# Performance work log

Hardware: AMD Instinct MI355X
Metric: run time of the kernel (lower is better)

Reference implementation:

```python
import jax, jax.numpy as jnp
import numpy as np

NUM_IT = 5            # init_kwargs num_it
N_NODES = 200_000
N_EDGES = 6_400_000   # avg degree 32
N_INIT_COLORS = 16

# odd 32-bit mixing constants (Knuth / xxhash primes); uint32 mults wrap mod 2^32
M1 = np.uint32(2654435761)
M2 = np.uint32(2246822519)
M3 = np.uint32(3266489917)
M4 = np.uint32(668265263)


def setup_inputs() -> dict:
    key = jax.random.key(0)
    k1, k2 = jax.random.split(key)
    x = jax.random.randint(k1, (N_NODES,), 0, N_INIT_COLORS, dtype=jnp.int32)
    edge_index = jax.random.randint(k2, (2, N_EDGES), 0, N_NODES, dtype=jnp.int32)
    return {"x": x, "edge_index": edge_index}


def _wl_iteration(colors, row, col, num_nodes):
    """One WLConv step: new color = id of (own color, sorted multiset of neighbor colors).

    The torch WLConv sorts each node's neighbor colors, hashes the tuple, and
    assigns compact ids via a dict. Here we do the same math vectorized:
    lexsort edges by (row, neighbor color), compute a position-weighted 2x32-bit
    hash of the sorted per-node sequence via segment_sum, mix in the node's own
    color, then relabel distinct keys to compact ids 0..k-1 with jnp.unique.
    """
    E = row.shape[0]
    c = colors[col]                                   # neighbor colors per edge [E]
    order = jnp.lexsort((c, row))                     # sort by node, then by color
    r_s = row[order]                                  # [E] sorted rows
    c_s = c[order].astype(jnp.uint32)                 # [E] sorted neighbor colors

    ones = jnp.ones((E,), dtype=jnp.int32)
    deg = jax.ops.segment_sum(ones, row, num_segments=num_nodes)      # [N]
    start = jnp.cumsum(deg) - deg                                     # segment offsets [N]
    pos = (jnp.arange(E, dtype=jnp.int32) - start[r_s]).astype(jnp.uint32)  # rank within node

    # two independent position-weighted hash lanes over each sorted neighbor list
    lane1 = jax.ops.segment_sum((c_s + 1) * (pos * M1 + M2), r_s, num_segments=num_nodes)
    lane2 = jax.ops.segment_sum((c_s + 1) * (pos * M3 + M4), r_s, num_segments=num_nodes)

    own = colors.astype(jnp.uint32) + 1
    key2 = jnp.stack([lane1 * M2 + own * M1, lane2 * M4 + own * M3], axis=1)  # [N,2]

    # dict-style relabeling: distinct keys -> compact ids (at most N distinct)
    _, inv = jnp.unique(key2, axis=0, size=num_nodes, return_inverse=True,
                        fill_value=jnp.uint32(0))
    return inv.reshape(-1).astype(colors.dtype)


def reference(x, edge_index):
    row, col = edge_index[0], edge_index[1]
    colors = x.astype(jnp.int32)
    for _ in range(NUM_IT):  # fixed small layer loop, not a data-dim loop
        colors = _wl_iteration(colors, row, col, N_NODES)
    return colors
```

## Files before the change

### kernel.cpp

```cpp
#include <hip/hip_runtime.h>
#include <stdint.h>

typedef unsigned int u32;
typedef unsigned long long u64;

#define M1 2654435761u
#define M2 2246822519u
#define M3 3266489917u
#define M4 668265263u
#define NUM_IT 5
#define PCHUNK 16384
#define HCH 65536
#define TILE 4096
#define PBCH 4096
#define CCAP 16384
#define SB 64
#define CHB 33
#define NKB 2048
#define KSH 53
#define KCH 4096
#define SCH 8192


__global__ void k_init(const int* __restrict__ x, int* __restrict__ colors,
                       u32* __restrict__ bcnt5, u32* __restrict__ bhist,
                       u32* __restrict__ cnt3, int n, int nbuck) {
    int i = blockIdx.x * blockDim.x + threadIdx.x;
    if (i < n) colors[i] = x[i];
    if (i < 2 * NUM_IT * NKB) bcnt5[i] = 0u;
    if (i >= 24576 && i < 24576 + nbuck) bhist[i - 24576] = 0u;
    if (i >= 32768 && i < 32768 + 48) cnt3[i - 32768] = 0u;
}

__global__ void k_chist(const int* __restrict__ row, u32* __restrict__ bhist,
                        u32* __restrict__ thist, int e, int nbuck) {
    __shared__ u32 fineh[1024];
    __shared__ u32 shist[16 * SB];
    int t = threadIdx.x;
    fineh[t] = 0u;
    shist[t] = 0u;
    __syncthreads();
    int c0 = blockIdx.x * HCH;
    int ce = c0 + HCH; if (ce > e) ce = e;
    int k = 0;
    for (int i = c0 + t; i < ce; i += 1024, ++k) {
        u32 r = (u32)row[i];
        atomicAdd(&fineh[r >> 8], 1u);
        atomicAdd(&shist[((k >> 2) << 6) | (r >> 12)], 1u);
    }
    __syncthreads();
    if (t < nbuck) {
        u32 v = fineh[t];
        if (v) atomicAdd(&bhist[t], v);
    }
    {
        int m = t >> 6;
        if (c0 + m * TILE < e)
            thist[(size_t)(blockIdx.x * 16 + m) * SB + (t & 63)] = shist[t];
    }
}

__global__ void k_cscan(const u32* __restrict__ bhist, u32* __restrict__ boffE,
                        u32* __restrict__ bcur, u32* __restrict__ boffS,
                        int nbuck, int nbS) {
    __shared__ u32 sh[256];
    u32 run = 0u;
    for (int base = 0; base < nbuck; base += 256) {
        int id = base + threadIdx.x;
        u32 x = (id < nbuck) ? bhist[id] : 0u;
        sh[threadIdx.x] = x;
        __syncthreads();
        for (int o = 1; o < 256; o <<= 1) {
            u32 t = (threadIdx.x >= (u32)o) ? sh[threadIdx.x - o] : 0u;
            __syncthreads();
            sh[threadIdx.x] += t;
            __syncthreads();
        }
        if (id < nbuck) {
            u32 excl = sh[threadIdx.x] - x + run;
            boffE[id] = excl;
            bcur[id] = excl;
            if ((id & 15) == 0) boffS[id >> 4] = excl;
        }
        u32 tot = sh[255];
        __syncthreads();
        run += tot;
    }
    if (threadIdx.x == 0) { boffE[nbuck] = run; boffS[nbS] = run; }
}

__global__ void k_tscan(const u32* __restrict__ thist, const u32* __restrict__ boffS,
                        u32* __restrict__ tbase, int ntiles) {
    __shared__ u32 sh[256];
    int b = blockIdx.x;
    int t = threadIdx.x;
    u32 run = boffS[b];
    for (int base = 0; base < ntiles; base += 256) {
        int tile = base + t;
        u32 x = (tile < ntiles) ? thist[(size_t)tile * SB + b] : 0u;
        sh[t] = x;
        __syncthreads();
        for (int o = 1; o < 256; o <<= 1) {
            u32 y = (t >= o) ? sh[t - o] : 0u;
            __syncthreads();
            sh[t] += y;
            __syncthreads();
        }
        if (tile < ntiles) tbase[(size_t)tile * SB + b] = run + sh[t] - x;
        u32 tot = sh[255];
        __syncthreads();
        run += tot;
    }
}

__global__ void k_partA(const int* __restrict__ row, const int* __restrict__ col,
                        const u32* __restrict__ thist, const u32* __restrict__ tbase,
                        u32* __restrict__ adjt, int e) {
    __shared__ u32 vals[TILE];
    __shared__ unsigned char bkt[TILE];
    __shared__ u32 lbase[SB + 1], gbase[SB], cur[SB];
    int t = threadIdx.x;
    int c0 = blockIdx.x * TILE;
    int ce = c0 + TILE; if (ce > e) ce = e;
    if (t < SB) {
        gbase[t] = tbase[(size_t)blockIdx.x * SB + t];
        cur[t] = 0u;
        lbase[t] = thist[(size_t)blockIdx.x * SB + t];
    }
    __syncthreads();
    if (t == 0) {
        u32 run = 0u;
        for (int b = 0; b < SB; ++b) { u32 h = lbase[b]; lbase[b] = run; run += h; }
        lbase[SB] = run;
    }
    __syncthreads();
    for (int i = c0 + t; i < ce; i += 256) {
        u32 r = (u32)row[i];
        u32 s = r >> 12;
        u32 p = lbase[s] + atomicAdd(&cur[s], 1u);
        vals[p] = ((r & 4095u) << 18) | (u32)col[i];
        bkt[p] = (unsigned char)s;
    }
    __syncthreads();
    int cnt = ce - c0;
    for (int i = t; i < cnt; i += 256) {
        u32 b = (u32)bkt[i];
        adjt[gbase[b] + ((u32)i - lbase[b])] = vals[i];
    }
}

__global__ void k_partB(const u32* __restrict__ adjt, const u32* __restrict__ boffS,
                        u32* __restrict__ ecur, u32* __restrict__ adj) {
    __shared__ u32 vals[PBCH];
    __shared__ u32 hist[16], lbase[17], gbase[16], cur[16];
    int s = blockIdx.x / CHB, c = blockIdx.x % CHB;
    u32 lo = boffS[s] + (u32)c * PBCH;
    u32 hi = boffS[s + 1];
    if (lo >= hi) return;
    if (hi > lo + PBCH) hi = lo + PBCH;
    int t = threadIdx.x;
    if (t < 16) hist[t] = 0u;
    __syncthreads();
    for (u32 i = lo + t; i < hi; i += 256)
        atomicAdd(&hist[(adjt[i] >> 26) & 15u], 1u);
    __syncthreads();
    if (t == 0) {
        u32 run = 0u;
        for (int b = 0; b < 16; ++b) { lbase[b] = run; run += hist[b]; }
        lbase[16] = run;
    }
    __syncthreads();
    if (t < 16) {
        u32 h = hist[t];
        gbase[t] = h ? atomicAdd(&ecur[s * 16 + t], h) : 0u;
        cur[t] = 0u;
    }
    __syncthreads();
    for (u32 i = lo + t; i < hi; i += 256) {
        u32 v = adjt[i];
        u32 b = (v >> 26) & 15u;
        vals[lbase[b] + atomicAdd(&cur[b], 1u)] = v;
    }
    __syncthreads();
    u32 cnt = hi - lo;
    for (u32 i = t; i < cnt; i += 256) {
        u32 v = vals[i];
        u32 b = (v >> 26) & 15u;
        adj[gbase[b] + (i - lbase[b])] = v & 0x03FFFFFFu;
    }
}

__global__ void k_part(const int* __restrict__ row, const int* __restrict__ col,
                       u32* __restrict__ bcur, u32* __restrict__ adjp, int e, int nbuck) {
    __shared__ u32 hist[1024], base[1024], cur[1024];
    int c0 = blockIdx.x * PCHUNK;
    int cend = c0 + PCHUNK; if (cend > e) cend = e;
    for (int t = threadIdx.x; t < nbuck; t += 256) hist[t] = 0u;
    __syncthreads();
    for (int i = c0 + threadIdx.x; i < cend; i += 256)
        atomicAdd(&hist[((u32)row[i]) >> 8], 1u);
    __syncthreads();
    for (int t = threadIdx.x; t < nbuck; t += 256) {
        u32 h = hist[t];
        base[t] = h ? atomicAdd(&bcur[t], h) : 0u;
        cur[t] = 0u;
    }
    __syncthreads();
    for (int i = c0 + threadIdx.x; i < cend; i += 256) {
        u32 r = (u32)row[i];
        u32 b = r >> 8;
        u32 local = atomicAdd(&cur[b], 1u);
        adjp[base[b] + local] = ((r & 255u) << 18) | (u32)col[i];
    }
}

__global__ void k_csr(u32* __restrict__ adj, const u32* __restrict__ boffE,
                      u32* __restrict__ deg, u32* __restrict__ start,
                      u64* __restrict__ lists, u32* __restrict__ cnt3, int n) {
    __shared__ u32 buf[CCAP];
    __shared__ u32 cnt[256], cur[256];
    __shared__ u32 wsum[4];
    __shared__ u32 ch[3], cbase[3];
    int b = blockIdx.x;
    int v0 = b << 8;
    u32 bs = boffE[b], be = boffE[b + 1];
    int c = (int)(be - bs);
    if (c > CCAP) c = CCAP;
    int t = threadIdx.x;
    int lane = t & 63, w = t >> 6;
    if (t < 256) cnt[t] = 0u;
    if (t < 3) ch[t] = 0u;
    for (int i = t; i < c; i += 1024) buf[i] = adj[bs + i];
    __syncthreads();
    for (int i = t; i < c; i += 1024)
        atomicAdd(&cnt[buf[i] >> 18], 1u);
    __syncthreads();
    u32 myc = 0u, ps = 0u;
    if (t < 256) {
        myc = cnt[t];
        ps = myc;
#pragma unroll
        for (int o = 1; o < 64; o <<= 1) {
            u32 y = (u32)__shfl_up((int)ps, o, 64);
            if (lane >= o) ps += y;
        }
        if (lane == 63) wsum[w] = ps;
    }
    __syncthreads();
    u32 cls = 0u, crk = 0u, myStart = 0u;
    int v = v0 + t;
    if (t < 256) {
        u32 wb = 0u;
        for (int j = 0; j < w; ++j) wb += wsum[j];
        u32 excl = wb + ps - myc;
        myStart = bs + excl;
        if (v < n) {
            deg[v] = myc;
            start[v] = myStart;
            cls = (myc <= 32u) ? 0u : ((myc <= 64u) ? 1u : 2u);
            crk = atomicAdd(&ch[cls], 1u);
        }
        cur[t] = myStart;
    }
    __syncthreads();
    if (t < 3) cbase[t] = ch[t] ? atomicAdd(&cnt3[t * 16], ch[t]) : 0u;
    __syncthreads();
    if (t < 256 && v < n) {
        u32 dcl = myc > 0x3FFFu ? 0x3FFFu : myc;
        lists[cls * (size_t)n + cbase[cls] + crk] =
            ((u64)((dcl << 18) | (u32)v) << 32) | (u64)myStart;
    }
    for (int i = t; i < c; i += 1024) {
        u32 p = buf[i];
        u32 q = atomicAdd(&cur[p >> 18], 1u);
        adj[q] = p & 0x3FFFFu;
    }
}


__device__ __forceinline__ void ce_reg(u32& a, u32& b, bool up) {
    u32 mn = a < b ? a : b, mx = a < b ? b : a;
    a = up ? mn : mx; b = up ? mx : mn;
}
__device__ __forceinline__ void ce_shf(u32& a, int o, bool tm) {
    u32 ot = (u32)__shfl_xor((int)a, o, 64);
    u32 mn = a < ot ? a : ot, mx = a < ot ? ot : a;
    a = tm ? mn : mx;
}
#define CE_SH4(o, tm) { ce_shf(c0, o, tm); ce_shf(c1, o, tm); ce_shf(c2, o, tm); ce_shf(c3, o, tm); }
#define CE_RG4(up)    { ce_reg(c0, c2, up); ce_reg(c1, c3, up); ce_reg(c0, c1, up); ce_reg(c2, c3, up); }

__global__ void k_hash(const int* __restrict__ colors, const u32* __restrict__ deg,
                       const u32* __restrict__ adj,
                       const u64* __restrict__ lists, const u32* __restrict__ cnt3,
                       u64* __restrict__ keys, int n) {
    int lane = threadIdx.x & 63;
    int wid = (int)((blockIdx.x * 256u + threadIdx.x) >> 6);
    u32 nA = cnt3[0], nBc = cnt3[16], nCc = cnt3[32];
    int octA = (int)((nA + 7u) >> 3);
    int quadB = (int)((nBc + 3u) >> 2);
    if (wid < octA) {
        int s = lane & 7;
        int li = 8 * wid + (lane >> 3);
        int node = -1;
        u32 c0 = 0xFFFFFFFFu, c1 = 0xFFFFFFFFu, c2 = 0xFFFFFFFFu, c3 = 0xFFFFFFFFu;
        u32 e0 = 4u * (u32)s;
        if (li < (int)nA) {
            u64 pk = lists[li];
            u32 st = (u32)pk;
            u32 hi = (u32)(pk >> 32);
            u32 d = hi >> 18;
            node = (int)(hi & 0x3FFFFu);
            if (e0 + 0u < d) c0 = (u32)colors[adj[st + e0 + 0u]];
            if (e0 + 1u < d) c1 = (u32)colors[adj[st + e0 + 1u]];
            if (e0 + 2u < d) c2 = (u32)colors[adj[st + e0 + 2u]];
            if (e0 + 3u < d) c3 = (u32)colors[adj[st + e0 + 3u]];
        }
        bool s1 = (s & 1) == 0, s2 = (s & 2) == 0, s4 = (s & 4) == 0;
        ce_reg(c0, c1, true); ce_reg(c2, c3, false);
        CE_RG4(s1)
        CE_SH4(1, s1 == s2)
        CE_RG4(s2)
        CE_SH4(2, s2 == s4)
        CE_SH4(1, s1 == s4)
        CE_RG4(s4)
        CE_SH4(4, s4)
        CE_SH4(2, s2)
        CE_SH4(1, s1)
        CE_RG4(true)
        u32 a1 = e0 * M1, a3 = e0 * M3;
        u32 v = (c0 + 1u) * (a1 + M2)           + (c1 + 1u) * (a1 + 1u * M1 + M2)
              + (c2 + 1u) * (a1 + 2u * M1 + M2) + (c3 + 1u) * (a1 + 3u * M1 + M2);
        u32 w = (c0 + 1u) * (a3 + M4)           + (c1 + 1u) * (a3 + 1u * M3 + M4)
              + (c2 + 1u) * (a3 + 2u * M3 + M4) + (c3 + 1u) * (a3 + 3u * M3 + M4);
#pragma unroll
        for (int o = 1; o < 8; o <<= 1) {
            v += (u32)__shfl_xor((int)v, o, 64);
            w += (u32)__shfl_xor((int)w, o, 64);
        }
        if (s == 0 && node >= 0) {
            u32 own = (u32)colors[node] + 1u;
            keys[node] = ((u64)(v * M2 + own * M1) << 32) | (u64)(w * M4 + own * M3);
        }
    } else if (wid < octA + quadB) {
        int s = lane & 15;
        int li = 4 * (wid - octA) + (lane >> 4);
        int node = -1;
        u32 c0 = 0xFFFFFFFFu, c1 = 0xFFFFFFFFu, c2 = 0xFFFFFFFFu, c3 = 0xFFFFFFFFu;
        u32 e0 = 4u * (u32)s;
        if (li < (int)nBc) {
            u64 pk = lists[(size_t)n + (u32)li];
            u32 st = (u32)pk;
            u32 hi = (u32)(pk >> 32);
            u32 d = hi >> 18;
            node = (int)(hi & 0x3FFFFu);
            if (e0 + 0u < d) c0 = (u32)colors[adj[st + e0 + 0u]];
            if (e0 + 1u < d) c1 = (u32)colors[adj[st + e0 + 1u]];
            if (e0 + 2u < d) c2 = (u32)colors[adj[st + e0 + 2u]];
            if (e0 + 3u < d) c3 = (u32)colors[adj[st + e0 + 3u]];
        }
        bool s1 = (s & 1) == 0, s2 = (s & 2) == 0, s4 = (s & 4) == 0, s8 = (s & 8) == 0;
        ce_reg(c0, c1, true); ce_reg(c2, c3, false);
        CE_RG4(s1)
        CE_SH4(1, s1 == s2)
        CE_RG4(s2)
        CE_SH4(2, s2 == s4)
        CE_SH4(1, s1 == s4)
        CE_RG4(s4)
        CE_SH4(4, s4 == s8)
        CE_SH4(2, s2 == s8)
        CE_SH4(1, s1 == s8)
        CE_RG4(s8)
        CE_SH4(8, s8)
        CE_SH4(4, s4)
        CE_SH4(2, s2)
        CE_SH4(1, s1)
        CE_RG4(true)
        u32 a1 = e0 * M1, a3 = e0 * M3;
        u32 v = (c0 + 1u) * (a1 + M2)           + (c1 + 1u) * (a1 + 1u * M1 + M2)
              + (c2 + 1u) * (a1 + 2u * M1 + M2) + (c3 + 1u) * (a1 + 3u * M1 + M2);
        u32 w = (c0 + 1u) * (a3 + M4)           + (c1 + 1u) * (a3 + 1u * M3 + M4)
              + (c2 + 1u) * (a3 + 2u * M3 + M4) + (c3 + 1u) * (a3 + 3u * M3 + M4);
#pragma unroll
        for (int o = 1; o < 16; o <<= 1) {
            v += (u32)__shfl_xor((int)v, o, 64);
            w += (u32)__shfl_xor((int)w, o, 64);
        }
        if (s == 0 && node >= 0) {
            u32 own = (u32)colors[node] + 1u;
            keys[node] = ((u64)(v * M2 + own * M1) << 32) | (u64)(w * M4 + own * M3);
        }
    } else if (wid < octA + quadB + (int)nCc) {
        u64 pk = lists[2u * (size_t)n + (u32)(wid - octA - quadB)];
        int node = (int)((u32)(pk >> 32) & 0x3FFFFu);
        u32 st = (u32)pk;
        u32 d = deg[node];
        u32 v = 0u, w = 0u;
        for (u32 i = (u32)lane; i < d; i += 64u) {
            u32 ci = (u32)colors[adj[st + i]];
            u32 pos = 0u;
            for (u32 j = 0; j < d; ++j) {
                u32 cj = (u32)colors[adj[st + j]];
                pos += (cj < ci) || (cj == ci && j < i);
            }
            v += (ci + 1u) * (pos * M1 + M2);
            w += (ci + 1u) * (pos * M3 + M4);
        }
        for (int o = 32; o > 0; o >>= 1) {
            v += (u32)__shfl_xor((int)v, o, 64);
            w += (u32)__shfl_xor((int)w, o, 64);
        }
        if (lane == 0) {
            u32 own = (u32)colors[node] + 1u;
            keys[node] = ((u64)(v * M2 + own * M1) << 32) | (u64)(w * M4 + own * M3);
        }
    }
}


__global__ void k_khist(const u64* __restrict__ keys, u32* __restrict__ bcnt, int n) {
    __shared__ u32 h[NKB];
    int t = threadIdx.x;
    for (int i = t; i < NKB; i += 256) h[i] = 0u;
    __syncthreads();
    int c0 = blockIdx.x * KCH;
    int ce = c0 + KCH; if (ce > n) ce = n;
    for (int i = c0 + t; i < ce; i += 256)
        atomicAdd(&h[(u32)(keys[i] >> KSH)], 1u);
    __syncthreads();
    for (int i = t; i < NKB; i += 256) {
        u32 v = h[i];
        if (v) atomicAdd(&bcnt[i], v);
    }
}

__global__ void k_scatter(const u64* __restrict__ keys, u64* __restrict__ out,
                          u32* __restrict__ nout, const u32* __restrict__ bcnt,
                          u32* __restrict__ cur, u32* __restrict__ boff, int n) {
    __shared__ u32 h[NKB], base[NKB], boffL[NKB];
    int t = threadIdx.x;
    h[t] = 0u; h[t + 1024] = 0u;
    if (t < 64) {
        u32 v[32]; u32 s = 0u;
#pragma unroll
        for (int i = 0; i < 32; ++i) { v[i] = bcnt[t * 32 + i]; s += v[i]; }
        u32 ps = s;
#pragma unroll
        for (int o = 1; o < 64; o <<= 1) {
            u32 y = (u32)__shfl_up((int)ps, o, 64);
            if (t >= o) ps += y;
        }
        u32 run = ps - s;
#pragma unroll
        for (int i = 0; i < 32; ++i) { boffL[t * 32 + i] = run; run += v[i]; }
    }
    __syncthreads();
    if (blockIdx.x == 0) {
        boff[t] = boffL[t];
        boff[t + 1024] = boffL[t + 1024];
        if (t == 0) boff[NKB] = boffL[NKB - 1] + bcnt[NKB - 1];
    }
    int c0 = blockIdx.x * SCH;
    u64 k[8]; u32 r[8];
#pragma unroll
    for (int i = 0; i < 8; ++i) {
        int id = c0 + t + i * 1024;
        if (id < n) { k[i] = keys[id]; r[i] = atomicAdd(&h[(u32)(k[i] >> KSH)], 1u); }
    }
    __syncthreads();
    base[t] = boffL[t] + (h[t] ? atomicAdd(&cur[t], h[t]) : 0u);
    base[t + 1024] = boffL[t + 1024] + (h[t + 1024] ? atomicAdd(&cur[t + 1024], h[t + 1024]) : 0u);
    __syncthreads();
#pragma unroll
    for (int i = 0; i < 8; ++i) {
        int id = c0 + t + i * 1024;
        if (id < n) {
            u32 p = base[(u32)(k[i] >> KSH)] + r[i];
            out[p] = k[i];
            nout[p] = (u32)id;
        }
    }
}

__global__ void k_bsort(u64* __restrict__ data, u32* __restrict__ nidx,
                        const u32* __restrict__ boff,
                        u32* __restrict__ comb, u32* __restrict__ dcount) {
    __shared__ u64 sh[256];
    __shared__ u32 pid[256];
    __shared__ u32 ts[256];
    int b = blockIdx.x;
    u32 lo = boff[b];
    int cnt = (int)(boff[b + 1] - lo);
    if (cnt > 256) cnt = 256;
    int m = (cnt <= 128) ? 128 : 256;
    int t = threadIdx.x;
    for (int i = t; i < m; i += 256) {
        sh[i] = (i < cnt) ? data[lo + i] : ~0ULL;
        pid[i] = (i < cnt) ? nidx[lo + i] : 0u;
    }
    __syncthreads();
    for (int k = 2; k <= m; k <<= 1) {
        for (int j = k >> 1; j > 0; j >>= 1) {
            for (int e = t; e < m; e += 256) {
                int p = e ^ j;
                if (p > e) {
                    u64 a = sh[e], c = sh[p];
                    bool up = ((e & k) == 0);
                    if (up ? (a > c) : (a < c)) {
                        sh[e] = c; sh[p] = a;
                        u32 tp = pid[e]; pid[e] = pid[p]; pid[p] = tp;
                    }
                }
            }
            __syncthreads();
        }
    }
    int i0 = 2 * t, i1 = 2 * t + 1;
    u32 f0 = (i0 < cnt) ? ((i0 == 0) ? 1u : (sh[i0] != sh[i0 - 1] ? 1u : 0u)) : 0u;
    u32 f1 = (i1 < cnt) ? (sh[i1] != sh[i1 - 1] ? 1u : 0u) : 0u;
    u32 s2 = f0 + f1;
    ts[t] = s2;
    __syncthreads();
    for (int o = 1; o < 256; o <<= 1) {
        u32 x = (t >= o) ? ts[t - o] : 0u;
        __syncthreads();
        ts[t] += x;
        __syncthreads();
    }
    u32 excl = ts[t] - s2;
    u32 tag = (u32)b << 16;
    if (i0 < cnt) { nidx[lo + i0] = pid[i0]; comb[lo + i0] = tag | (excl + f0); }
    if (i1 < cnt) { nidx[lo + i1] = pid[i1]; comb[lo + i1] = tag | (excl + f0 + f1); }
    if (t == 255) dcount[b] = ts[255];
}

__global__ void k_relabel(const u32* __restrict__ comb, const u32* __restrict__ nidx,
                          const u32* __restrict__ dcount, int* __restrict__ colors, int n) {
    __shared__ u32 dbaseL[NKB];
    int t = threadIdx.x;
    if (t < 64) {
        u32 v[32]; u32 s = 0u;
#pragma unroll
        for (int i = 0; i < 32; ++i) { v[i] = dcount[t * 32 + i]; s += v[i]; }
        u32 ps = s;
#pragma unroll
        for (int o = 1; o < 64; o <<= 1) {
            u32 y = (u32)__shfl_up((int)ps, o, 64);
            if (t >= o) ps += y;
        }
        u32 run = ps - s;
#pragma unroll
        for (int i = 0; i < 32; ++i) { dbaseL[t * 32 + i] = run; run += v[i]; }
    }
    __syncthreads();
    int i = blockIdx.x * 256 + t;
    if (i >= n) return;
    u32 c = comb[i];
    colors[nidx[i]] = (int)(dbaseL[c >> 16] + (c & 0xFFFFu) - 1u);
}


extern "C" void kernel_launch(void* const* d_in, const int* in_sizes, int n_in,
                              void* d_out, int out_size, void* d_ws, size_t ws_size,
                              hipStream_t stream) {
    const int* x = (const int*)d_in[0];
    const int* ei = (const int*)d_in[1];
    const int N = in_sizes[0];
    const int E = in_sizes[1] / 2;
    const int* row = ei;
    const int* col = ei + E;
    int* colors = (int*)d_out;

    const int ntiles = (E + TILE - 1) / TILE;

    char* ws = (char*)d_ws;
    size_t off = 0;
#define WS_ALLOC(T, name, bytes) T name = (T)(ws + off); off += (((size_t)(bytes)) + 255) & ~(size_t)255;
    WS_ALLOC(u32*, deg, (size_t)N * 4)
    WS_ALLOC(u32*, start, (size_t)N * 4)
    WS_ALLOC(u32*, adj, (size_t)E * 4)
    WS_ALLOC(u64*, keys, (size_t)N * 8)
    WS_ALLOC(u64*, sorted, (size_t)N * 8)
    WS_ALLOC(u32*, nidx, (size_t)N * 4)
    WS_ALLOC(u32*, comb, (size_t)N * 4)
    WS_ALLOC(u64*, lists, (size_t)3 * N * 8)
    WS_ALLOC(u32*, bcnt5, (size_t)2 * NUM_IT * NKB * 4)
    WS_ALLOC(u32*, boff, (NKB + 1) * 4)
    WS_ALLOC(u32*, dcount, NKB * 4)
    WS_ALLOC(u32*, bhist, 1024 * 4)
    WS_ALLOC(u32*, boffE, 1025 * 4)
    WS_ALLOC(u32*, bcur, 1024 * 4)
    WS_ALLOC(u32*, boffS, (SB + 1) * 4)
    WS_ALLOC(u32*, cnt3, 48 * 4)
    WS_ALLOC(u32*, thist, (size_t)ntiles * SB * 4)
    WS_ALLOC(u32*, tbase, (size_t)ntiles * SB * 4)
    u32* adjt = (u32*)(ws + off);
    const bool two_level = (off + (size_t)E * 4 <= ws_size);
#undef WS_ALLOC

    const int nB = (N + 255) / 256;
    const int nbuck = (N + 255) >> 8;
    const int nbS = (nbuck + 15) >> 4;
    const int kB = (N + KCH - 1) / KCH;
    const int sBk = (N + SCH - 1) / SCH;

    k_init<<<nB, 256, 0, stream>>>(x, colors, bcnt5, bhist, cnt3, N, nbuck);
    k_chist<<<(E + HCH - 1) / HCH, 1024, 0, stream>>>(row, bhist, thist, E, nbuck);
    k_cscan<<<1, 256, 0, stream>>>(bhist, boffE, bcur, boffS, nbuck, nbS);
    if (two_level) {
        k_tscan<<<nbS, 256, 0, stream>>>(thist, boffS, tbase, ntiles);
        k_partA<<<ntiles, 256, 0, stream>>>(row, col, thist, tbase, adjt, E);
        k_partB<<<nbS * CHB, 256, 0, stream>>>(adjt, boffS, bcur, adj);
    } else {
        k_part<<<(E + PCHUNK - 1) / PCHUNK, 256, 0, stream>>>(row, col, bcur, adj, E, nbuck);
    }
    k_csr<<<nbuck, 1024, 0, stream>>>(adj, boffE, deg, start, lists, cnt3, N);

    for (int it = 0; it < NUM_IT; ++it) {
        u32* bcnt = bcnt5 + it * NKB;
        u32* bcur_it = bcnt5 + (NUM_IT + it) * NKB;
        k_hash<<<(N + 3) / 4, 256, 0, stream>>>(colors, deg, adj, lists, cnt3, keys, N);
        k_khist<<<kB, 256, 0, stream>>>(keys, bcnt, N);
        k_scatter<<<sBk, 1024, 0, stream>>>(keys, sorted, nidx, bcnt, bcur_it, boff, N);
        k_bsort<<<NKB, 256, 0, stream>>>(sorted, nidx, boff, comb, dcount);
        k_relabel<<<nB, 256, 0, stream>>>(comb, nidx, dcount, colors, N);
    }
}
```

Measured before the change: 631.6 us.

## Replace histogram+prefix scatter with fixed-slot bucket scatter and per-bucket relabel

Drops the separate key histogram kernel and the prefix-sum-based scatter. Keys are now scattered into fixed 256-entry slots per top-bit bucket using one global atomic counter per bucket, padded to 64 bytes to avoid false sharing. Relabel becomes one block per bucket that reduces the preceding dcount entries itself. This saves a launch per iteration and the scan work, but it silently drops keys if any bucket exceeds 256 entries (the old code also capped at 256), and the relabel reduction is quadratic across buckets.

```diff
diff --git a/kernel.cpp b/kernel.cpp
--- a/kernel.cpp
+++ b/kernel.cpp
@@ -18,18 +18,17 @@
 #define CHB 33
 #define NKB 2048
 #define KSH 53
-#define KCH 4096
-#define SCH 8192
+#define SLOT 256
 
 
 __global__ void k_init(const int* __restrict__ x, int* __restrict__ colors,
-                       u32* __restrict__ bcnt5, u32* __restrict__ bhist,
+                       u32* __restrict__ cnt5, u32* __restrict__ bhist,
                        u32* __restrict__ cnt3, int n, int nbuck) {
     int i = blockIdx.x * blockDim.x + threadIdx.x;
     if (i < n) colors[i] = x[i];
-    if (i < 2 * NUM_IT * NKB) bcnt5[i] = 0u;
-    if (i >= 24576 && i < 24576 + nbuck) bhist[i - 24576] = 0u;
-    if (i >= 32768 && i < 32768 + 48) cnt3[i - 32768] = 0u;
+    if (i < NUM_IT * NKB * 16) cnt5[i] = 0u;
+    if (i >= 165888 && i < 165888 + nbuck) bhist[i - 165888] = 0u;
+    if (i >= 168960 && i < 168960 + 48) cnt3[i - 168960] = 0u;
 }
 
 __global__ void k_chist(const int* __restrict__ row, u32* __restrict__ bhist,
@@ -418,85 +417,35 @@
 }
 
 
-__global__ void k_khist(const u64* __restrict__ keys, u32* __restrict__ bcnt, int n) {
-    __shared__ u32 h[NKB];
-    int t = threadIdx.x;
-    for (int i = t; i < NKB; i += 256) h[i] = 0u;
-    __syncthreads();
-    int c0 = blockIdx.x * KCH;
-    int ce = c0 + KCH; if (ce > n) ce = n;
-    for (int i = c0 + t; i < ce; i += 256)
-        atomicAdd(&h[(u32)(keys[i] >> KSH)], 1u);
-    __syncthreads();
-    for (int i = t; i < NKB; i += 256) {
-        u32 v = h[i];
-        if (v) atomicAdd(&bcnt[i], v);
-    }
-}
-
 __global__ void k_scatter(const u64* __restrict__ keys, u64* __restrict__ out,
-                          u32* __restrict__ nout, const u32* __restrict__ bcnt,
-                          u32* __restrict__ cur, u32* __restrict__ boff, int n) {
-    __shared__ u32 h[NKB], base[NKB], boffL[NKB];
-    int t = threadIdx.x;
-    h[t] = 0u; h[t + 1024] = 0u;
-    if (t < 64) {
-        u32 v[32]; u32 s = 0u;
-#pragma unroll
-        for (int i = 0; i < 32; ++i) { v[i] = bcnt[t * 32 + i]; s += v[i]; }
-        u32 ps = s;
-#pragma unroll
-        for (int o = 1; o < 64; o <<= 1) {
-            u32 y = (u32)__shfl_up((int)ps, o, 64);
-            if (t >= o) ps += y;
-        }
-        u32 run = ps - s;
-#pragma unroll
-        for (int i = 0; i < 32; ++i) { boffL[t * 32 + i] = run; run += v[i]; }
-    }
-    __syncthreads();
-    if (blockIdx.x == 0) {
-        boff[t] = boffL[t];
-        boff[t + 1024] = boffL[t + 1024];
-        if (t == 0) boff[NKB] = boffL[NKB - 1] + bcnt[NKB - 1];
-    }
-    int c0 = blockIdx.x * SCH;
-    u64 k[8]; u32 r[8];
-#pragma unroll
-    for (int i = 0; i < 8; ++i) {
-        int id = c0 + t + i * 1024;
-        if (id < n) { k[i] = keys[id]; r[i] = atomicAdd(&h[(u32)(k[i] >> KSH)], 1u); }
-    }
-    __syncthreads();
-    base[t] = boffL[t] + (h[t] ? atomicAdd(&cur[t], h[t]) : 0u);
-    base[t + 1024] = boffL[t + 1024] + (h[t + 1024] ? atomicAdd(&cur[t + 1024], h[t + 1024]) : 0u);
-    __syncthreads();
-#pragma unroll
-    for (int i = 0; i < 8; ++i) {
-        int id = c0 + t + i * 1024;
-        if (id < n) {
-            u32 p = base[(u32)(k[i] >> KSH)] + r[i];
-            out[p] = k[i];
-            nout[p] = (u32)id;
-        }
+                          u32* __restrict__ nout, u32* __restrict__ cnt, int n) {
+    int i = blockIdx.x * 256 + threadIdx.x;
+    if (i >= n) return;
+    u64 k = keys[i];
+    u32 b = (u32)(k >> KSH);
+    u32 r = atomicAdd(&cnt[b * 16], 1u);
+    if (r < (u32)SLOT) {
+        u32 p = (b << 8) + r;
+        out[p] = k;
+        nout[p] = (u32)i;
     }
 }
 
 __global__ void k_bsort(u64* __restrict__ data, u32* __restrict__ nidx,
-                        const u32* __restrict__ boff,
+                        const u32* __restrict__ cnt,
                         u32* __restrict__ comb, u32* __restrict__ dcount) {
     __shared__ u64 sh[256];
     __shared__ u32 pid[256];
     __shared__ u32 ts[256];
     int b = blockIdx.x;
-    u32 lo = boff[b];
-    int cnt = (int)(boff[b + 1] - lo);
-    if (cnt > 256) cnt = 256;
-    int m = (cnt <= 128) ? 128 : 256;
+    u32 lo = (u32)b << 8;
+    int c = (int)cnt[b * 16];
+    if (c > SLOT) c = SLOT;
+    int m = (c <= 128) ? 128 : 256;
     int t = threadIdx.x;
     for (int i = t; i < m; i += 256) {
-        sh[i] = (i < cnt) ? data[lo + i] : ~0ULL;
-        pid[i] = (i < cnt) ? nidx[lo + i] : 0u;
+        sh[i] = (i < c) ? data[lo + i] : ~0ULL;
+        pid[i] = (i < c) ? nidx[lo + i] : 0u;
     }
     __syncthreads();
     for (int k = 2; k <= m; k <<= 1) {
@@ -504,10 +453,10 @@
             for (int e = t; e < m; e += 256) {
                 int p = e ^ j;
                 if (p > e) {
-                    u64 a = sh[e], c = sh[p];
+                    u64 a = sh[e], cc = sh[p];
                     bool up = ((e & k) == 0);
-                    if (up ? (a > c) : (a < c)) {
-                        sh[e] = c; sh[p] = a;
+                    if (up ? (a > cc) : (a < cc)) {
+                        sh[e] = cc; sh[p] = a;
                         u32 tp = pid[e]; pid[e] = pid[p]; pid[p] = tp;
                     }
                 }
@@ -516,8 +465,8 @@
         }
     }
     int i0 = 2 * t, i1 = 2 * t + 1;
-    u32 f0 = (i0 < cnt) ? ((i0 == 0) ? 1u : (sh[i0] != sh[i0 - 1] ? 1u : 0u)) : 0u;
-    u32 f1 = (i1 < cnt) ? (sh[i1] != sh[i1 - 1] ? 1u : 0u) : 0u;
+    u32 f0 = (i0 < c) ? ((i0 == 0) ? 1u : (sh[i0] != sh[i0 - 1] ? 1u : 0u)) : 0u;
+    u32 f1 = (i1 < c) ? (sh[i1] != sh[i1 - 1] ? 1u : 0u) : 0u;
     u32 s2 = f0 + f1;
     ts[t] = s2;
     __syncthreads();
@@ -528,35 +477,31 @@
         __syncthreads();
     }
     u32 excl = ts[t] - s2;
-    u32 tag = (u32)b << 16;
-    if (i0 < cnt) { nidx[lo + i0] = pid[i0]; comb[lo + i0] = tag | (excl + f0); }
-    if (i1 < cnt) { nidx[lo + i1] = pid[i1]; comb[lo + i1] = tag | (excl + f0 + f1); }
+    if (i0 < c) { nidx[lo + i0] = pid[i0]; comb[lo + i0] = excl + f0; }
+    if (i1 < c) { nidx[lo + i1] = pid[i1]; comb[lo + i1] = excl + f0 + f1; }
     if (t == 255) dcount[b] = ts[255];
 }
 
 __global__ void k_relabel(const u32* __restrict__ comb, const u32* __restrict__ nidx,
-                          const u32* __restrict__ dcount, int* __restrict__ colors, int n) {
-    __shared__ u32 dbaseL[NKB];
-    int t = threadIdx.x;
-    if (t < 64) {
-        u32 v[32]; u32 s = 0u;
-#pragma unroll
-        for (int i = 0; i < 32; ++i) { v[i] = dcount[t * 32 + i]; s += v[i]; }
-        u32 ps = s;
-#pragma unroll
-        for (int o = 1; o < 64; o <<= 1) {
-            u32 y = (u32)__shfl_up((int)ps, o, 64);
-            if (t >= o) ps += y;
-        }
-        u32 run = ps - s;
-#pragma unroll
-        for (int i = 0; i < 32; ++i) { dbaseL[t * 32 + i] = run; run += v[i]; }
-    }
-    __syncthreads();
-    int i = blockIdx.x * 256 + t;
-    if (i >= n) return;
-    u32 c = comb[i];
-    colors[nidx[i]] = (int)(dbaseL[c >> 16] + (c & 0xFFFFu) - 1u);
+                          const u32* __restrict__ dcount, const u32* __restrict__ cnt,
+                          int* __restrict__ colors) {
+    __shared__ u32 red[256];
+    int b = blockIdx.x;
+    int t = threadIdx.x;
+    u32 partial = 0u;
+    for (int j = t; j < b; j += 256) partial += dcount[j];
+    red[t] = partial;
+    __syncthreads();
+    for (int o = 128; o > 0; o >>= 1) {
+        if (t < o) red[t] += red[t + o];
+        __syncthreads();
+    }
+    u32 dbase = red[0];
+    u32 c = cnt[b * 16];
+    if (c > (u32)SLOT) c = (u32)SLOT;
+    u32 lo = (u32)b << 8;
+    for (u32 i = (u32)t; i < c; i += 256u)
+        colors[nidx[lo + i]] = (int)(dbase + comb[lo + i] - 1u);
 }
 
 
@@ -580,12 +525,11 @@
     WS_ALLOC(u32*, start, (size_t)N * 4)
     WS_ALLOC(u32*, adj, (size_t)E * 4)
     WS_ALLOC(u64*, keys, (size_t)N * 8)
-    WS_ALLOC(u64*, sorted, (size_t)N * 8)
-    WS_ALLOC(u32*, nidx, (size_t)N * 4)
-    WS_ALLOC(u32*, comb, (size_t)N * 4)
+    WS_ALLOC(u64*, sorted, (size_t)NKB * SLOT * 8)
+    WS_ALLOC(u32*, nidx, (size_t)NKB * SLOT * 4)
+    WS_ALLOC(u32*, comb, (size_t)NKB * SLOT * 4)
     WS_ALLOC(u64*, lists, (size_t)3 * N * 8)
-    WS_ALLOC(u32*, bcnt5, (size_t)2 * NUM_IT * NKB * 4)
-    WS_ALLOC(u32*, boff, (NKB + 1) * 4)
+    WS_ALLOC(u32*, cnt5, (size_t)NUM_IT * NKB * 16 * 4)
     WS_ALLOC(u32*, dcount, NKB * 4)
     WS_ALLOC(u32*, bhist, 1024 * 4)
     WS_ALLOC(u32*, boffE, 1025 * 4)
@@ -601,10 +545,8 @@
     const int nB = (N + 255) / 256;
     const int nbuck = (N + 255) >> 8;
     const int nbS = (nbuck + 15) >> 4;
-    const int kB = (N + KCH - 1) / KCH;
-    const int sBk = (N + SCH - 1) / SCH;
-
-    k_init<<<nB, 256, 0, stream>>>(x, colors, bcnt5, bhist, cnt3, N, nbuck);
+
+    k_init<<<nB, 256, 0, stream>>>(x, colors, cnt5, bhist, cnt3, N, nbuck);
     k_chist<<<(E + HCH - 1) / HCH, 1024, 0, stream>>>(row, bhist, thist, E, nbuck);
     k_cscan<<<1, 256, 0, stream>>>(bhist, boffE, bcur, boffS, nbuck, nbS);
     if (two_level) {
@@ -617,12 +559,10 @@
     k_csr<<<nbuck, 1024, 0, stream>>>(adj, boffE, deg, start, lists, cnt3, N);
 
     for (int it = 0; it < NUM_IT; ++it) {
-        u32* bcnt = bcnt5 + it * NKB;
-        u32* bcur_it = bcnt5 + (NUM_IT + it) * NKB;
+        u32* cnt_it = cnt5 + (size_t)it * NKB * 16;
         k_hash<<<(N + 3) / 4, 256, 0, stream>>>(colors, deg, adj, lists, cnt3, keys, N);
-        k_khist<<<kB, 256, 0, stream>>>(keys, bcnt, N);
-        k_scatter<<<sBk, 1024, 0, stream>>>(keys, sorted, nidx, bcnt, bcur_it, boff, N);
-        k_bsort<<<NKB, 256, 0, stream>>>(sorted, nidx, boff, comb, dcount);
-        k_relabel<<<nB, 256, 0, stream>>>(comb, nidx, dcount, colors, N);
-    }
-}
+        k_scatter<<<nB, 256, 0, stream>>>(keys, sorted, nidx, cnt_it, N);
+        k_bsort<<<NKB, 256, 0, stream>>>(sorted, nidx, cnt_it, comb, dcount);
+        k_relabel<<<NKB, 256, 0, stream>>>(comb, nidx, dcount, cnt_it, colors);
+    }
+}
```

Measured after the change: 594.6 us, median of 2. 5.8% less time.
